# Kernel optimization log

Measured on AMD Instinct MI355X. Metric: run time of the kernel, lower is better.

The kernel has to match this reference:

```python
import jax, jax.numpy as jnp
import numpy as np
import math

B, S, D, H, L, F = 32, 512, 512, 8, 4, 2048
DK = D // H
EPS = 1e-5


def _cosine_pos_emb(seq_len, d_model):
    pe = np.zeros((seq_len, d_model), dtype=np.float32)
    position = np.arange(seq_len, dtype=np.float32)[:, None]
    div_term = np.exp(np.arange(0, d_model, 2, dtype=np.float32) * (-math.log(10000.0) / d_model))
    pe[:, 0::2] = np.sin(position * div_term)
    pe[:, 1::2] = np.cos(position * div_term)
    return jnp.asarray(pe[None])  # (1, S, D)


def setup_inputs() -> dict:
    key = jax.random.key(0)
    ks = jax.random.split(key, 12)
    w = 0.02
    return {
        "q_embed_data": jax.random.normal(ks[0], (B, S, D), jnp.float32),
        "qa_embed_data": jax.random.normal(ks[1], (B, S, D), jnp.float32),
        "forget_rate": jax.random.uniform(ks[2], (B, S, 1), jnp.float32),
        "pos_emb": _cosine_pos_emb(S, D),
        # per-layer stacked params (torch Linear convention: W is (out,in))
        "Wk": w * jax.random.normal(ks[3], (L, D, D), jnp.float32),
        "bk": jnp.zeros((L, D), jnp.float32),
        "Wv": w * jax.random.normal(ks[4], (L, D, D), jnp.float32),
        "bv": jnp.zeros((L, D), jnp.float32),
        "Wo": w * jax.random.normal(ks[5], (L, D, D), jnp.float32),
        "bo": jnp.zeros((L, D), jnp.float32),
        "W1": w * jax.random.normal(ks[6], (L, F, D), jnp.float32),
        "b1": jnp.zeros((L, F), jnp.float32),
        "W2": w * jax.random.normal(ks[7], (L, D, F), jnp.float32),
        "b2": jnp.zeros((L, D), jnp.float32),
        "ln1_g": jnp.ones((L, D), jnp.float32),
        "ln1_b": jnp.zeros((L, D), jnp.float32),
        "ln2_g": jnp.ones((L, D), jnp.float32),
        "ln2_b": jnp.zeros((L, D), jnp.float32),
    }


def _layer_norm(x, g, b):
    mu = jnp.mean(x, axis=-1, keepdims=True)
    var = jnp.mean(jnp.square(x - mu), axis=-1, keepdims=True)
    return (x - mu) * jax.lax.rsqrt(var + EPS) * g + b


def _forward(q_embed_data, qa_embed_data, forget_rate, pos_emb,
             Wk, bk, Wv, bv, Wo, bo, W1, b1, W2, b2,
             ln1_g, ln1_b, ln2_g, ln2_b):
    x = q_embed_data + pos_emb   # queries/keys stream
    y = qa_embed_data + pos_emb  # values stream (fixed across layers)
    scale = 1.0 / math.sqrt(DK)
    # mask=0 path: triu(k=0)==0 -> strictly past positions only (j < i)
    allowed = jnp.tril(jnp.ones((S, S), dtype=bool), k=-1)
    fr = forget_rate[:, None, :, :]  # (B,1,S,1): row-wise decay on scores
    neg = jnp.asarray(-1e32, x.dtype)

    def block(x, p):
        wk, bk_, wv, bv_, wo, bo_, w1, b1_, w2, b2_, g1, be1, g2, be2 = p
        # kq_same=1: q and k share the k_linear projection (so q == k here)
        kq = (jnp.einsum('bsd,ed->bse', x, wk) + bk_).reshape(B, S, H, DK).transpose(0, 2, 1, 3)
        v = (jnp.einsum('bsd,ed->bse', y, wv) + bv_).reshape(B, S, H, DK).transpose(0, 2, 1, 3)
        scores = jnp.einsum('bhsd,bhtd->bhst', kq, kq) * scale
        scores = scores * fr
        scores = jnp.where(allowed, scores, neg)
        attn = jax.nn.softmax(scores, axis=-1)
        attn = attn.at[:, :, 0, :].set(0.0)  # zero_pad: first query row zeroed
        ctx = jnp.einsum('bhst,bhtd->bhsd', attn, v).transpose(0, 2, 1, 3).reshape(B, S, D)
        out = jnp.einsum('bsd,ed->bse', ctx, wo) + bo_
        x = _layer_norm(x + out, g1, be1)
        ff = jnp.einsum('bsf,df->bsd', jax.nn.relu(jnp.einsum('bsd,fd->bsf', x, w1) + b1_), w2) + b2_
        x = _layer_norm(x + ff, g2, be2)
        return x, None

    x, _ = jax.lax.scan(block, x, (Wk, bk, Wv, bv, Wo, bo, W1, b1, W2, b2, ln1_g, ln1_b, ln2_g, ln2_b))
    return x


def reference(q_embed_data, qa_embed_data, forget_rate, pos_emb,
              Wk, bk, Wv, bv, Wo, bo, W1, b1, W2, b2,
              ln1_g, ln1_b, ln2_g, ln2_b):
    return _forward(q_embed_data, qa_embed_data, forget_rate, pos_emb,
                    Wk, bk, Wv, bv, Wo, bo, W1, b1, W2, b2,
                    ln1_g, ln1_b, ln2_g, ln2_b)
```

## Files before the change

### kernel.cpp

```cpp
#include <hip/hip_runtime.h>
#include <hip/hip_bf16.h>

constexpr int B_ = 32, S_ = 512, D_ = 512, H_ = 8, L_ = 4, F_ = 2048, DK_ = 64;

typedef __attribute__((ext_vector_type(8))) short short8;
typedef __attribute__((ext_vector_type(4))) float f32x4;

__device__ inline unsigned short f2b(float f) {
  union { __hip_bfloat16 h; unsigned short u; } cv;
  cv.h = __float2bfloat16(f);
  return cv.u;
}
__device__ inline float b2f(unsigned short u) {
  union { unsigned int i; float f; } c;
  c.i = ((unsigned int)u) << 16;
  return c.f;
}
__device__ inline float waveReduceSum(float v) {
  #pragma unroll
  for (int o = 32; o > 0; o >>= 1) v += __shfl_xor(v, o);
  return v;
}

__global__ void prep_kernel(const float4* __restrict__ q, const float4* __restrict__ qa,
                            const float4* __restrict__ pos, float4* __restrict__ xf,
                            uint2* __restrict__ xb, uint2* __restrict__ yb) {
  int i = blockIdx.x * blockDim.x + threadIdx.x;
  float4 p = pos[i & 65535];
  float4 a = q[i], c = qa[i];
  float4 xv, yv;
  xv.x = a.x + p.x; xv.y = a.y + p.y; xv.z = a.z + p.z; xv.w = a.w + p.w;
  yv.x = c.x + p.x; yv.y = c.y + p.y; yv.z = c.z + p.z; yv.w = c.w + p.w;
  xf[i] = xv;
  uint2 px, py;
  px.x = (unsigned)f2b(xv.x) | ((unsigned)f2b(xv.y) << 16);
  px.y = (unsigned)f2b(xv.z) | ((unsigned)f2b(xv.w) << 16);
  py.x = (unsigned)f2b(yv.x) | ((unsigned)f2b(yv.y) << 16);
  py.y = (unsigned)f2b(yv.z) | ((unsigned)f2b(yv.w) << 16);
  xb[i] = px;
  yb[i] = py;
}

__global__ void cast_kernel(const float4* __restrict__ src, uint2* __restrict__ dst, int n4) {
  int i = blockIdx.x * blockDim.x + threadIdx.x;
  if (i >= n4) return;
  float4 v = src[i];
  uint2 p;
  p.x = (unsigned)f2b(v.x) | ((unsigned)f2b(v.y) << 16);
  p.y = (unsigned)f2b(v.z) | ((unsigned)f2b(v.w) << 16);
  dst[i] = p;
}

template<int RELU, int STORE>
__global__ __launch_bounds__(256, 2) void gemm128_kernel(
    const __hip_bfloat16* __restrict__ A,
    const __hip_bfloat16* __restrict__ W,
    const float* __restrict__ bias,
    const __hip_bfloat16* __restrict__ A2,
    const __hip_bfloat16* __restrict__ W2,
    const float* __restrict__ bias2,
    __hip_bfloat16* __restrict__ Cb,
    __hip_bfloat16* __restrict__ Cb2,
    int Ndim, int Kdim, int kLen)
{
  __shared__ char lds[32768];
  const int tid = threadIdx.x, wave = tid >> 6, lane = tid & 63;
  const int rl = lane & 15, gq = lane >> 4;
  const int wr = wave >> 1, wc = wave & 1;

  const int nwg = gridDim.x * gridDim.y;
  const int lin = blockIdx.y * gridDim.x + blockIdx.x;
  const int swz = (lin & 7) * (nwg >> 3) + (lin >> 3);
  const int bx = swz % gridDim.x, by = swz / gridDim.x;

  const int row0 = by * 128;
  const int col0 = bx * 128;

  const __hip_bfloat16* Ap = A;
  const __hip_bfloat16* Wp = W;
  const float* bp = bias;
  int kOff = blockIdx.z * kLen;
  if (STORE == 3) {
    kOff = 0;
    if (blockIdx.z) { Ap = A2; Wp = W2; bp = bias2; }
  }

  f32x4 acc[4][4] = {};
  const int ntiles = kLen >> 5;

  auto stage = [&](int kt, int d) {
    const int kbase = kOff + (kt << 5);
    #pragma unroll
    for (int r = 0; r < 2; ++r) {
      int p = r * 4096 + tid * 16;
      int R = p >> 6, c = (p >> 4) & 3;
      int gc = c ^ ((R >> 1) & 3);
      const __hip_bfloat16* srcA = Ap + (size_t)(row0 + R) * Kdim + kbase + gc * 8;
      __builtin_amdgcn_global_load_lds(
          (const __attribute__((address_space(1))) void*)srcA,
          (__attribute__((address_space(3))) void*)(lds + d * 8192 + p), 16, 0, 0);
      const __hip_bfloat16* srcW = Wp + (size_t)(col0 + R) * Kdim + kbase + gc * 8;
      __builtin_amdgcn_global_load_lds(
          (const __attribute__((address_space(1))) void*)srcW,
          (__attribute__((address_space(3))) void*)(lds + 16384 + d * 8192 + p), 16, 0, 0);
    }
  };

  stage(0, 0);
  __syncthreads();
  for (int kt = 0; kt < ntiles; ++kt) {
    const int d = kt & 1;
    if (kt + 1 < ntiles) stage(kt + 1, d ^ 1);

    short8 aF[4], bF[4];
    #pragma unroll
    for (int m = 0; m < 4; ++m) {
      int rr = wr * 64 + m * 16 + rl;
      aF[m] = *(const short8*)(lds + d * 8192 + rr * 64 + ((gq ^ ((rr >> 1) & 3)) << 4));
    }
    #pragma unroll
    for (int n = 0; n < 4; ++n) {
      int rr = wc * 64 + n * 16 + rl;
      bF[n] = *(const short8*)(lds + 16384 + d * 8192 + rr * 64 + ((gq ^ ((rr >> 1) & 3)) << 4));
    }
    __builtin_amdgcn_s_setprio(1);
    #pragma unroll
    for (int m = 0; m < 4; ++m)
      #pragma unroll
      for (int n = 0; n < 4; ++n)
        acc[m][n] = __builtin_amdgcn_mfma_f32_16x16x32_bf16(aF[m], bF[n], acc[m][n], 0, 0, 0);
    __builtin_amdgcn_s_setprio(0);
    __syncthreads();
  }

  char* sw = lds + wave * 8192;
  const bool vt = (STORE == 3) && (blockIdx.z == 1);
  const bool addb = (STORE == 3) ? true : ((bias != nullptr) && (blockIdx.z == 0));
  float bvv[4];
  #pragma unroll
  for (int n = 0; n < 4; ++n)
    bvv[n] = addb ? bp[col0 + wc * 64 + n * 16 + rl] : 0.0f;

  #pragma unroll
  for (int n = 0; n < 4; ++n)
    #pragma unroll
    for (int m = 0; m < 4; ++m)
      #pragma unroll
      for (int j = 0; j < 4; ++j) {
        float val = acc[m][n][j] + bvv[n];
        if (RELU) val = fmaxf(val, 0.0f);
        int addr;
        if (vt) {
          int orow = n * 16 + rl, ocol = m * 16 + gq * 4 + j;
          addr = orow * 128 + ((ocol * 2) ^ ((orow & 7) << 4));
        } else {
          int orow = m * 16 + gq * 4 + j;
          addr = orow * 128 + (((n * 16 + rl) * 2) ^ (((orow >> 1) & 7) << 4));
        }
        *(unsigned short*)(sw + addr) = f2b(val);
      }
  asm volatile("s_waitcnt lgkmcnt(0)" ::: "memory");
  __builtin_amdgcn_sched_barrier(0);

  __hip_bfloat16* Cbd = blockIdx.z ? Cb2 : Cb;
  const int cchunk = lane & 7;
  if (vt) {
    const int bh64 = ((row0 >> 9) * 8 + (col0 >> 6) + wc) * 64;
    const int tbase = (row0 & 511) + wr * 64;
    #pragma unroll
    for (int it = 0; it < 8; ++it) {
      int d0 = it * 8 + (lane >> 3);
      uint4 vv = *(const uint4*)(sw + d0 * 128 + ((cchunk * 16) ^ ((d0 & 7) << 4)));
      *(uint4*)((char*)Cbd + ((size_t)(bh64 + d0) * 512 + tbase) * 2 + cchunk * 16) = vv;
    }
  } else {
    #pragma unroll
    for (int it = 0; it < 8; ++it) {
      int orow = it * 8 + (lane >> 3);
      uint4 vv = *(const uint4*)(sw + orow * 128 + ((cchunk * 16) ^ (((orow >> 1) & 7) << 4)));
      *(uint4*)((char*)Cbd + ((size_t)(row0 + wr * 64 + orow) * Ndim + col0 + wc * 64) * 2 +
                cchunk * 16) = vv;
    }
  }
}

__global__ __launch_bounds__(256, 2) void fattn_kernel(
    const __hip_bfloat16* __restrict__ kq,
    const __hip_bfloat16* __restrict__ vT,
    const float* __restrict__ fr,
    __hip_bfloat16* __restrict__ ctx)
{
  __shared__ char lds[40960];
  const int tid = threadIdx.x, wave = tid >> 6, lane = tid & 63;
  const int rl = lane & 15, gq = lane >> 4;
  const int lin = blockIdx.x;
  const int qb = (3 - (lin >> 8)) * 128;
  const int wpi = lin & 255;
  const int bh = (wpi & 7) * 32 + (wpi >> 3);
  const int b = bh >> 3, h = bh & 7;
  const size_t kqbase = ((size_t)b * S_) * D_ + h * DK_;
  const size_t vtbase = ((size_t)bh * DK_) * S_;
  const int qw0 = qb + wave * 32;
  const int qw_end = qw0 + 32;

  short8 qA[2][2];
  #pragma unroll
  for (int qf = 0; qf < 2; ++qf)
    #pragma unroll
    for (int kf = 0; kf < 2; ++kf)
      qA[qf][kf] = *(const short8*)(kq + kqbase + (size_t)(qw0 + qf * 16 + rl) * D_ + kf * 32 + gq * 8);

  float sfv[2][4];
  #pragma unroll
  for (int qf = 0; qf < 2; ++qf)
    #pragma unroll
    for (int j = 0; j < 4; ++j)
      sfv[qf][j] = fr[b * S_ + qw0 + qf * 16 + gq * 4 + j] * 0.125f;

  f32x4 o[2][4] = {};
  float mrow[2][4], lrow[2][4];
  #pragma unroll
  for (int qf = 0; qf < 2; ++qf)
    #pragma unroll
    for (int j = 0; j < 4; ++j) { mrow[qf][j] = -3.0e38f; lrow[qf][j] = 0.0f; }

  int sgoff[2], sldsoff[2];
  #pragma unroll
  for (int c = 0; c < 2; ++c) {
    int p = (wave * 2 + c) * 1024 + lane * 16;
    int r = p >> 7;
    int ch = (p >> 4) & 7;
    sgoff[c] = r * 1024 + ((ch ^ (r & 7)) << 4);
    sldsoff[c] = (wave * 2 + c) * 1024;
  }
  const char* kgbase = (const char*)kq + kqbase * 2;
  const char* vgbase = (const char*)vT + vtbase * 2;

  auto stage = [&](int ti, int d) {
    const int t0 = ti << 6;
    #pragma unroll
    for (int c = 0; c < 2; ++c) {
      __builtin_amdgcn_global_load_lds(
          (const __attribute__((address_space(1))) void*)(kgbase + (size_t)t0 * 1024 + sgoff[c]),
          (__attribute__((address_space(3))) void*)(lds + d * 8192 + sldsoff[c]), 16, 0, 0);
      __builtin_amdgcn_global_load_lds(
          (const __attribute__((address_space(1))) void*)(vgbase + t0 * 2 + sgoff[c]),
          (__attribute__((address_space(3))) void*)(lds + 16384 + d * 8192 + sldsoff[c]), 16, 0, 0);
    }
  };

  const int nt = (qb + 128) >> 6;
  stage(0, 0);
  for (int ti = 0; ti < nt; ++ti) {
    const int t0 = ti << 6;
    const int d = ti & 1;
    if (ti + 1 < nt) {
      stage(ti + 1, d ^ 1);
      asm volatile("s_waitcnt vmcnt(4)" ::: "memory");
    } else {
      asm volatile("s_waitcnt vmcnt(0)" ::: "memory");
    }
    __builtin_amdgcn_sched_barrier(0);
    __builtin_amdgcn_s_barrier();
    __builtin_amdgcn_sched_barrier(0);

    if (t0 < qw_end) {
      short8 kB[4][2];
      #pragma unroll
      for (int tf = 0; tf < 4; ++tf)
        #pragma unroll
        for (int kf = 0; kf < 2; ++kf) {
          int r = tf * 16 + rl;
          kB[tf][kf] = *(const short8*)(lds + d * 8192 + r * 128 + (((kf * 4 + gq) ^ (r & 7)) << 4));
        }
      short8 vB[4][2];
      #pragma unroll
      for (int df = 0; df < 4; ++df)
        #pragma unroll
        for (int kf = 0; kf < 2; ++kf) {
          int r = df * 16 + rl;
          vB[df][kf] = *(const short8*)(lds + 16384 + d * 8192 + r * 128 + (((kf * 4 + gq) ^ (r & 7)) << 4));
        }

      #pragma unroll
      for (int qf = 0; qf < 2; ++qf) {
        f32x4 c4[4] = {};
        #pragma unroll
        for (int tf = 0; tf < 4; ++tf)
          #pragma unroll
          for (int kf = 0; kf < 2; ++kf)
            c4[tf] = __builtin_amdgcn_mfma_f32_16x16x32_bf16(qA[qf][kf], kB[tf][kf], c4[tf], 0, 0, 0);

        const int qg0 = qw0 + qf * 16 + gq * 4;
        #pragma unroll
        for (int tf = 0; tf < 4; ++tf) {
          int tg = t0 + tf * 16 + rl;
          #pragma unroll
          for (int j = 0; j < 4; ++j) {
            float s = c4[tf][j] * sfv[qf][j];
            c4[tf][j] = (tg >= qg0 + j) ? -3.0e38f : s;
          }
        }
        float tm[4];
        #pragma unroll
        for (int j = 0; j < 4; ++j) {
          tm[j] = fmaxf(fmaxf(c4[0][j], c4[1][j]), fmaxf(c4[2][j], c4[3][j]));
          #pragma unroll
          for (int msk = 1; msk < 16; msk <<= 1) tm[j] = fmaxf(tm[j], __shfl_xor(tm[j], msk));
        }
        #pragma unroll
        for (int j = 0; j < 4; ++j) {
          float mn = fmaxf(mrow[qf][j], tm[j]);
          float fac = __expf(mrow[qf][j] - mn);
          mrow[qf][j] = mn;
          lrow[qf][j] *= fac;
          #pragma unroll
          for (int df = 0; df < 4; ++df) o[qf][df][j] *= fac;
        }
        float rs[4] = {0.f, 0.f, 0.f, 0.f};
        #pragma unroll
        for (int tf = 0; tf < 4; ++tf) {
          int tloc = tf * 16 + rl;
          #pragma unroll
          for (int j = 0; j < 4; ++j) {
            float e = __expf(c4[tf][j] - mrow[qf][j]);
            rs[j] += e;
            int qloc = gq * 4 + j;
            int addr = 32768 + wave * 2048 + qloc * 128 +
                       ((((tloc >> 3) ^ (qloc & 7)) << 4)) + (tloc & 7) * 2;
            *(unsigned short*)(lds + addr) = f2b(e);
          }
        }
        #pragma unroll
        for (int j = 0; j < 4; ++j) {
          float r = rs[j];
          #pragma unroll
          for (int msk = 1; msk < 16; msk <<= 1) r += __shfl_xor(r, msk);
          lrow[qf][j] += r;
        }
        asm volatile("s_waitcnt lgkmcnt(0)" ::: "memory");
        __builtin_amdgcn_sched_barrier(0);
        short8 pA[2];
        #pragma unroll
        for (int kf = 0; kf < 2; ++kf)
          pA[kf] = *(const short8*)(lds + 32768 + wave * 2048 + rl * 128 +
                                    (((kf * 4 + gq) ^ (rl & 7)) << 4));
        #pragma unroll
        for (int df = 0; df < 4; ++df)
          #pragma unroll
          for (int kf = 0; kf < 2; ++kf)
            o[qf][df] = __builtin_amdgcn_mfma_f32_16x16x32_bf16(pA[kf], vB[df][kf], o[qf][df], 0, 0, 0);
      }
    }
    __builtin_amdgcn_sched_barrier(0);
    __builtin_amdgcn_s_barrier();
    __builtin_amdgcn_sched_barrier(0);
  }

  #pragma unroll
  for (int qf = 0; qf < 2; ++qf)
    #pragma unroll
    for (int j = 0; j < 4; ++j) {
      int qg = qw0 + qf * 16 + gq * 4 + j;
      float inv = (qg == 0) ? 0.0f : 1.0f / lrow[qf][j];
      #pragma unroll
      for (int df = 0; df < 4; ++df) {
        union { __hip_bfloat16 hh; unsigned short u; } cv;
        cv.u = f2b(o[qf][df][j] * inv);
        ctx[((size_t)(b * S_ + qg)) * D_ + h * DK_ + df * 16 + rl] = cv.hh;
      }
    }
}

template<int NADD>
__global__ __launch_bounds__(256) void ln_kernel(
    const float4* __restrict__ xin, const uint4* __restrict__ add,
    const uint4* __restrict__ add2,
    const float* __restrict__ g, const float* __restrict__ bta,
    float4* xf_out, uint2* __restrict__ xb_out)
{
  const int lane = threadIdx.x & 63, wv = threadIdx.x >> 6;
  const size_t row = (size_t)blockIdx.x * 4 + wv;
  const size_t base4 = row * 128;

  float4 x0 = xin[base4 + lane * 2], x1 = xin[base4 + lane * 2 + 1];
  uint4 ab = add[row * 64 + lane];
  const unsigned short* ap = (const unsigned short*)&ab;
  float v[8];
  v[0] = x0.x; v[1] = x0.y; v[2] = x0.z; v[3] = x0.w;
  v[4] = x1.x; v[5] = x1.y; v[6] = x1.z; v[7] = x1.w;
  #pragma unroll
  for (int i = 0; i < 8; ++i) v[i] += b2f(ap[i]);
  if (NADD == 2) {
    uint4 ab2 = add2[row * 64 + lane];
    const unsigned short* ap2 = (const unsigned short*)&ab2;
    #pragma unroll
    for (int i = 0; i < 8; ++i) v[i] += b2f(ap2[i]);
  }
  float s = 0.0f;
  #pragma unroll
  for (int i = 0; i < 8; ++i) s += v[i];
  s = waveReduceSum(s);
  float mu = s * (1.0f / 512.0f);
  float vs = 0.0f;
  #pragma unroll
  for (int i = 0; i < 8; ++i) { float dd = v[i] - mu; vs += dd * dd; }
  vs = waveReduceSum(vs);
  float rstd = rsqrtf(vs * (1.0f / 512.0f) + 1e-5f);

  const int c0i = lane * 8;
  float4 gg0 = *(const float4*)(g + c0i), gg1 = *(const float4*)(g + c0i + 4);
  float4 bb0 = *(const float4*)(bta + c0i), bb1 = *(const float4*)(bta + c0i + 4);
  float o[8];
  o[0] = (v[0] - mu) * rstd * gg0.x + bb0.x;
  o[1] = (v[1] - mu) * rstd * gg0.y + bb0.y;
  o[2] = (v[2] - mu) * rstd * gg0.z + bb0.z;
  o[3] = (v[3] - mu) * rstd * gg0.w + bb0.w;
  o[4] = (v[4] - mu) * rstd * gg1.x + bb1.x;
  o[5] = (v[5] - mu) * rstd * gg1.y + bb1.y;
  o[6] = (v[6] - mu) * rstd * gg1.z + bb1.z;
  o[7] = (v[7] - mu) * rstd * gg1.w + bb1.w;
  float4 w0, w1;
  w0.x = o[0]; w0.y = o[1]; w0.z = o[2]; w0.w = o[3];
  w1.x = o[4]; w1.y = o[5]; w1.z = o[6]; w1.w = o[7];
  xf_out[base4 + lane * 2] = w0;
  xf_out[base4 + lane * 2 + 1] = w1;
  uint2 p0, p1;
  p0.x = (unsigned)f2b(o[0]) | ((unsigned)f2b(o[1]) << 16);
  p0.y = (unsigned)f2b(o[2]) | ((unsigned)f2b(o[3]) << 16);
  p1.x = (unsigned)f2b(o[4]) | ((unsigned)f2b(o[5]) << 16);
  p1.y = (unsigned)f2b(o[6]) | ((unsigned)f2b(o[7]) << 16);
  xb_out[row * 128 + lane * 2] = p0;
  xb_out[row * 128 + lane * 2 + 1] = p1;
}

extern "C" void kernel_launch(void* const* d_in, const int* in_sizes, int n_in,
                              void* d_out, int out_size, void* d_ws, size_t ws_size,
                              hipStream_t stream) {
  (void)in_sizes; (void)n_in; (void)out_size; (void)ws_size;
  const float* q   = (const float*)d_in[0];
  const float* qa  = (const float*)d_in[1];
  const float* frr = (const float*)d_in[2];
  const float* pos = (const float*)d_in[3];
  const float* Wk  = (const float*)d_in[4];
  const float* bk  = (const float*)d_in[5];
  const float* Wv  = (const float*)d_in[6];
  const float* bv  = (const float*)d_in[7];
  const float* Wo  = (const float*)d_in[8];
  const float* bo  = (const float*)d_in[9];
  const float* W1  = (const float*)d_in[10];
  const float* b1  = (const float*)d_in[11];
  const float* W2  = (const float*)d_in[12];
  const float* b2  = (const float*)d_in[13];
  const float* g1  = (const float*)d_in[14];
  const float* be1 = (const float*)d_in[15];
  const float* g2  = (const float*)d_in[16];
  const float* be2 = (const float*)d_in[17];

  char* ws = (char*)d_ws;
  float*          xf   = (float*)(ws + 0);
  __hip_bfloat16* xb   = (__hip_bfloat16*)(ws + 33554432);
  __hip_bfloat16* yb   = (__hip_bfloat16*)(ws + 50331648);
  __hip_bfloat16* kqb  = (__hip_bfloat16*)(ws + 67108864);
  __hip_bfloat16* vtb  = (__hip_bfloat16*)(ws + 83886080);
  __hip_bfloat16* ctxb = (__hip_bfloat16*)(ws + 100663296);
  __hip_bfloat16* hb   = (__hip_bfloat16*)(ws + 117440512);
  __hip_bfloat16* wkb  = (__hip_bfloat16*)(ws + 184549376);
  __hip_bfloat16* wvb  = (__hip_bfloat16*)(ws + 186646528);
  __hip_bfloat16* wob  = (__hip_bfloat16*)(ws + 188743680);
  __hip_bfloat16* w1b  = (__hip_bfloat16*)(ws + 190840832);
  __hip_bfloat16* w2b  = (__hip_bfloat16*)(ws + 199229440);
  __hip_bfloat16* obf = (__hip_bfloat16*)(ws + 67108864);
  __hip_bfloat16* pf0 = (__hip_bfloat16*)(ws + 83886080);
  __hip_bfloat16* pf1 = (__hip_bfloat16*)(ws + 100663296);

  prep_kernel<<<8192, 256, 0, stream>>>((const float4*)q, (const float4*)qa,
                                        (const float4*)pos, (float4*)xf,
                                        (uint2*)xb, (uint2*)yb);
  cast_kernel<<<1024, 256, 0, stream>>>((const float4*)Wk, (uint2*)wkb, 262144);
  cast_kernel<<<1024, 256, 0, stream>>>((const float4*)Wv, (uint2*)wvb, 262144);
  cast_kernel<<<1024, 256, 0, stream>>>((const float4*)Wo, (uint2*)wob, 262144);
  cast_kernel<<<4096, 256, 0, stream>>>((const float4*)W1, (uint2*)w1b, 1048576);
  cast_kernel<<<4096, 256, 0, stream>>>((const float4*)W2, (uint2*)w2b, 1048576);

  for (int l = 0; l < L_; ++l) {
    gemm128_kernel<0,3><<<dim3(4, 128, 2), 256, 0, stream>>>(
        xb, wkb + (size_t)l * 262144, bk + l * 512,
        yb, wvb + (size_t)l * 262144, bv + l * 512,
        kqb, vtb, 512, 512, 512);
    fattn_kernel<<<1024, 256, 0, stream>>>(kqb, vtb, frr, ctxb);
    gemm128_kernel<0,0><<<dim3(4, 128, 1), 256, 0, stream>>>(
        ctxb, wob + (size_t)l * 262144, bo + l * 512,
        nullptr, nullptr, nullptr, obf, nullptr, 512, 512, 512);
    ln_kernel<1><<<4096, 256, 0, stream>>>((const float4*)xf, (const uint4*)obf, nullptr,
                                           g1 + l * 512, be1 + l * 512,
                                           (float4*)xf, (uint2*)xb);
    gemm128_kernel<1,0><<<dim3(16, 128, 1), 256, 0, stream>>>(
        xb, w1b + (size_t)l * 1048576, b1 + l * 2048,
        nullptr, nullptr, nullptr, hb, nullptr, 2048, 512, 512);
    gemm128_kernel<0,0><<<dim3(4, 128, 2), 256, 0, stream>>>(
        hb, w2b + (size_t)l * 1048576, b2 + l * 512,
        nullptr, nullptr, nullptr, pf0, pf1, 512, 2048, 1024);
    float* lnout = (l == L_ - 1) ? (float*)d_out : xf;
    ln_kernel<2><<<4096, 256, 0, stream>>>((const float4*)xf, (const uint4*)pf0,
                                           (const uint4*)pf1,
                                           g2 + l * 512, be2 + l * 512,
                                           (float4*)lnout, (uint2*)xb);
  }
}
```

Before: 848.6 us.

## Load full per-head K and V into LDS and drop per-tile staging barriers

Each attention block now handles one (batch, head) half with 8 waves and loads that head's whole K and V (128 KB) into LDS once. The double-buffered per-tile staging and the block barriers inside the key loop are gone, and queries are read from LDS instead of global memory. Waves are assigned query strips in a mirrored order so that short and long causal rows share a block. The change removes repeated staging and synchronisation. In exchange, the 144 KB LDS footprint limits each CU to one block, so occupancy drops. All loads also happen up front with no overlap against compute, and the lower-query block loads K and V rows it never uses.

```diff
diff --git a/kernel.cpp b/kernel.cpp
--- a/kernel.cpp
+++ b/kernel.cpp
@@ -184,31 +184,43 @@
   }
 }
 
-__global__ __launch_bounds__(256, 2) void fattn_kernel(
+__global__ __launch_bounds__(512, 2) void fattn_kernel(
     const __hip_bfloat16* __restrict__ kq,
     const __hip_bfloat16* __restrict__ vT,
     const float* __restrict__ fr,
     __hip_bfloat16* __restrict__ ctx)
 {
-  __shared__ char lds[40960];
+  __shared__ char lds[147456];
   const int tid = threadIdx.x, wave = tid >> 6, lane = tid & 63;
   const int rl = lane & 15, gq = lane >> 4;
-  const int lin = blockIdx.x;
-  const int qb = (3 - (lin >> 8)) * 128;
-  const int wpi = lin & 255;
-  const int bh = (wpi & 7) * 32 + (wpi >> 3);
+  const int bh = blockIdx.x & 255;
+  const int blk = blockIdx.x >> 8;
   const int b = bh >> 3, h = bh & 7;
   const size_t kqbase = ((size_t)b * S_) * D_ + h * DK_;
   const size_t vtbase = ((size_t)bh * DK_) * S_;
-  const int qw0 = qb + wave * 32;
-  const int qw_end = qw0 + 32;
-
-  short8 qA[2][2];
-  #pragma unroll
-  for (int qf = 0; qf < 2; ++qf)
-    #pragma unroll
-    for (int kf = 0; kf < 2; ++kf)
-      qA[qf][kf] = *(const short8*)(kq + kqbase + (size_t)(qw0 + qf * 16 + rl) * D_ + kf * 32 + gq * 8);
+  const char* kg = (const char*)kq + kqbase * 2;
+  const char* vg = (const char*)vT + vtbase * 2;
+
+  #pragma unroll
+  for (int i = 0; i < 8; ++i) {
+    int p = i * 8192 + tid * 16;
+    int r = p >> 7, ch = (p >> 4) & 7;
+    __builtin_amdgcn_global_load_lds(
+        (const __attribute__((address_space(1))) void*)(kg + (size_t)r * 1024 + ((ch ^ (r & 7)) << 4)),
+        (__attribute__((address_space(3))) void*)(lds + p), 16, 0, 0);
+  }
+  #pragma unroll
+  for (int i = 0; i < 8; ++i) {
+    int p = i * 8192 + tid * 16;
+    int d = p >> 10, ck = (p >> 4) & 63;
+    __builtin_amdgcn_global_load_lds(
+        (const __attribute__((address_space(1))) void*)(vg + (size_t)d * 1024 + ((ck ^ (d & 7)) << 4)),
+        (__attribute__((address_space(3))) void*)(lds + 65536 + p), 16, 0, 0);
+  }
+
+  const int qidx = blk * 8 + (wave < 4 ? wave : 11 - wave);
+  const int qw0 = qidx * 32;
+  const int nt = (qidx >> 1) + 1;
 
   float sfv[2][4];
   #pragma unroll
@@ -217,6 +229,19 @@
     for (int j = 0; j < 4; ++j)
       sfv[qf][j] = fr[b * S_ + qw0 + qf * 16 + gq * 4 + j] * 0.125f;
 
+  asm volatile("s_waitcnt vmcnt(0)" ::: "memory");
+  __builtin_amdgcn_sched_barrier(0);
+  __builtin_amdgcn_s_barrier();
+
+  short8 qA[2][2];
+  #pragma unroll
+  for (int qf = 0; qf < 2; ++qf)
+    #pragma unroll
+    for (int kf = 0; kf < 2; ++kf) {
+      int r = qw0 + qf * 16 + rl;
+      qA[qf][kf] = *(const short8*)(lds + r * 128 + (((kf * 4 + gq) ^ (r & 7)) << 4));
+    }
+
   f32x4 o[2][4] = {};
   float mrow[2][4], lrow[2][4];
   #pragma unroll
@@ -224,137 +249,95 @@
     #pragma unroll
     for (int j = 0; j < 4; ++j) { mrow[qf][j] = -3.0e38f; lrow[qf][j] = 0.0f; }
 
-  int sgoff[2], sldsoff[2];
-  #pragma unroll
-  for (int c = 0; c < 2; ++c) {
-    int p = (wave * 2 + c) * 1024 + lane * 16;
-    int r = p >> 7;
-    int ch = (p >> 4) & 7;
-    sgoff[c] = r * 1024 + ((ch ^ (r & 7)) << 4);
-    sldsoff[c] = (wave * 2 + c) * 1024;
-  }
-  const char* kgbase = (const char*)kq + kqbase * 2;
-  const char* vgbase = (const char*)vT + vtbase * 2;
-
-  auto stage = [&](int ti, int d) {
-    const int t0 = ti << 6;
-    #pragma unroll
-    for (int c = 0; c < 2; ++c) {
-      __builtin_amdgcn_global_load_lds(
-          (const __attribute__((address_space(1))) void*)(kgbase + (size_t)t0 * 1024 + sgoff[c]),
-          (__attribute__((address_space(3))) void*)(lds + d * 8192 + sldsoff[c]), 16, 0, 0);
-      __builtin_amdgcn_global_load_lds(
-          (const __attribute__((address_space(1))) void*)(vgbase + t0 * 2 + sgoff[c]),
-          (__attribute__((address_space(3))) void*)(lds + 16384 + d * 8192 + sldsoff[c]), 16, 0, 0);
-    }
-  };
-
-  const int nt = (qb + 128) >> 6;
-  stage(0, 0);
+  char* pbase = lds + 131072 + wave * 2048;
+
   for (int ti = 0; ti < nt; ++ti) {
     const int t0 = ti << 6;
-    const int d = ti & 1;
-    if (ti + 1 < nt) {
-      stage(ti + 1, d ^ 1);
-      asm volatile("s_waitcnt vmcnt(4)" ::: "memory");
-    } else {
-      asm volatile("s_waitcnt vmcnt(0)" ::: "memory");
-    }
-    __builtin_amdgcn_sched_barrier(0);
-    __builtin_amdgcn_s_barrier();
-    __builtin_amdgcn_sched_barrier(0);
-
-    if (t0 < qw_end) {
-      short8 kB[4][2];
+    short8 kB[4][2];
+    #pragma unroll
+    for (int tf = 0; tf < 4; ++tf)
+      #pragma unroll
+      for (int kf = 0; kf < 2; ++kf) {
+        int r = t0 + tf * 16 + rl;
+        kB[tf][kf] = *(const short8*)(lds + r * 128 + (((kf * 4 + gq) ^ (r & 7)) << 4));
+      }
+    short8 vB[4][2];
+    #pragma unroll
+    for (int df = 0; df < 4; ++df)
+      #pragma unroll
+      for (int kf = 0; kf < 2; ++kf) {
+        int d = df * 16 + rl;
+        vB[df][kf] = *(const short8*)(lds + 65536 + d * 1024 +
+                                      ((8 * ti + ((kf * 4 + gq) ^ (d & 7))) << 4));
+      }
+
+    #pragma unroll
+    for (int qf = 0; qf < 2; ++qf) {
+      f32x4 c4[4] = {};
       #pragma unroll
       for (int tf = 0; tf < 4; ++tf)
         #pragma unroll
-        for (int kf = 0; kf < 2; ++kf) {
-          int r = tf * 16 + rl;
-          kB[tf][kf] = *(const short8*)(lds + d * 8192 + r * 128 + (((kf * 4 + gq) ^ (r & 7)) << 4));
+        for (int kf = 0; kf < 2; ++kf)
+          c4[tf] = __builtin_amdgcn_mfma_f32_16x16x32_bf16(qA[qf][kf], kB[tf][kf], c4[tf], 0, 0, 0);
+
+      const int qg0 = qw0 + qf * 16 + gq * 4;
+      #pragma unroll
+      for (int tf = 0; tf < 4; ++tf) {
+        int tg = t0 + tf * 16 + rl;
+        #pragma unroll
+        for (int j = 0; j < 4; ++j) {
+          float s = c4[tf][j] * sfv[qf][j];
+          c4[tf][j] = (tg >= qg0 + j) ? -3.0e38f : s;
         }
-      short8 vB[4][2];
+      }
+      float tm[4];
+      #pragma unroll
+      for (int j = 0; j < 4; ++j) {
+        tm[j] = fmaxf(fmaxf(c4[0][j], c4[1][j]), fmaxf(c4[2][j], c4[3][j]));
+        #pragma unroll
+        for (int msk = 1; msk < 16; msk <<= 1) tm[j] = fmaxf(tm[j], __shfl_xor(tm[j], msk));
+      }
+      #pragma unroll
+      for (int j = 0; j < 4; ++j) {
+        float mn = fmaxf(mrow[qf][j], tm[j]);
+        float fac = __expf(mrow[qf][j] - mn);
+        mrow[qf][j] = mn;
+        lrow[qf][j] *= fac;
+        #pragma unroll
+        for (int df = 0; df < 4; ++df) o[qf][df][j] *= fac;
+      }
+      float rs[4] = {0.f, 0.f, 0.f, 0.f};
+      #pragma unroll
+      for (int tf = 0; tf < 4; ++tf) {
+        int tloc = tf * 16 + rl;
+        #pragma unroll
+        for (int j = 0; j < 4; ++j) {
+          float e = __expf(c4[tf][j] - mrow[qf][j]);
+          rs[j] += e;
+          int qloc = gq * 4 + j;
+          int addr = qloc * 128 + ((((tloc >> 3) ^ (qloc & 7)) << 4)) + (tloc & 7) * 2;
+          *(unsigned short*)(pbase + addr) = f2b(e);
+        }
+      }
+      #pragma unroll
+      for (int j = 0; j < 4; ++j) {
+        float r = rs[j];
+        #pragma unroll
+        for (int msk = 1; msk < 16; msk <<= 1) r += __shfl_xor(r, msk);
+        lrow[qf][j] += r;
+      }
+      asm volatile("s_waitcnt lgkmcnt(0)" ::: "memory");
+      __builtin_amdgcn_sched_barrier(0);
+      short8 pA[2];
+      #pragma unroll
+      for (int kf = 0; kf < 2; ++kf)
+        pA[kf] = *(const short8*)(pbase + rl * 128 + (((kf * 4 + gq) ^ (rl & 7)) << 4));
       #pragma unroll
       for (int df = 0; df < 4; ++df)
         #pragma unroll
-        for (int kf = 0; kf < 2; ++kf) {
-          int r = df * 16 + rl;
-          vB[df][kf] = *(const short8*)(lds + 16384 + d * 8192 + r * 128 + (((kf * 4 + gq) ^ (r & 7)) << 4));
-        }
-
-      #pragma unroll
-      for (int qf = 0; qf < 2; ++qf) {
-        f32x4 c4[4] = {};
-        #pragma unroll
-        for (int tf = 0; tf < 4; ++tf)
-          #pragma unroll
-          for (int kf = 0; kf < 2; ++kf)
-            c4[tf] = __builtin_amdgcn_mfma_f32_16x16x32_bf16(qA[qf][kf], kB[tf][kf], c4[tf], 0, 0, 0);
-
-        const int qg0 = qw0 + qf * 16 + gq * 4;
-        #pragma unroll
-        for (int tf = 0; tf < 4; ++tf) {
-          int tg = t0 + tf * 16 + rl;
-          #pragma unroll
-          for (int j = 0; j < 4; ++j) {
-            float s = c4[tf][j] * sfv[qf][j];
-            c4[tf][j] = (tg >= qg0 + j) ? -3.0e38f : s;
-          }
-        }
-        float tm[4];
-        #pragma unroll
-        for (int j = 0; j < 4; ++j) {
-          tm[j] = fmaxf(fmaxf(c4[0][j], c4[1][j]), fmaxf(c4[2][j], c4[3][j]));
-          #pragma unroll
-          for (int msk = 1; msk < 16; msk <<= 1) tm[j] = fmaxf(tm[j], __shfl_xor(tm[j], msk));
-        }
-        #pragma unroll
-        for (int j = 0; j < 4; ++j) {
-          float mn = fmaxf(mrow[qf][j], tm[j]);
-          float fac = __expf(mrow[qf][j] - mn);
-          mrow[qf][j] = mn;
-          lrow[qf][j] *= fac;
-          #pragma unroll
-          for (int df = 0; df < 4; ++df) o[qf][df][j] *= fac;
-        }
-        float rs[4] = {0.f, 0.f, 0.f, 0.f};
-        #pragma unroll
-        for (int tf = 0; tf < 4; ++tf) {
-          int tloc = tf * 16 + rl;
-          #pragma unroll
-          for (int j = 0; j < 4; ++j) {
-            float e = __expf(c4[tf][j] - mrow[qf][j]);
-            rs[j] += e;
-            int qloc = gq * 4 + j;
-            int addr = 32768 + wave * 2048 + qloc * 128 +
-                       ((((tloc >> 3) ^ (qloc & 7)) << 4)) + (tloc & 7) * 2;
-            *(unsigned short*)(lds + addr) = f2b(e);
-          }
-        }
-        #pragma unroll
-        for (int j = 0; j < 4; ++j) {
-          float r = rs[j];
-          #pragma unroll
-          for (int msk = 1; msk < 16; msk <<= 1) r += __shfl_xor(r, msk);
-          lrow[qf][j] += r;
-        }
-        asm volatile("s_waitcnt lgkmcnt(0)" ::: "memory");
-        __builtin_amdgcn_sched_barrier(0);
-        short8 pA[2];
-        #pragma unroll
         for (int kf = 0; kf < 2; ++kf)
-          pA[kf] = *(const short8*)(lds + 32768 + wave * 2048 + rl * 128 +
-                                    (((kf * 4 + gq) ^ (rl & 7)) << 4));
-        #pragma unroll
-        for (int df = 0; df < 4; ++df)
-          #pragma unroll
-          for (int kf = 0; kf < 2; ++kf)
-            o[qf][df] = __builtin_amdgcn_mfma_f32_16x16x32_bf16(pA[kf], vB[df][kf], o[qf][df], 0, 0, 0);
-      }
-    }
-    __builtin_amdgcn_sched_barrier(0);
-    __builtin_amdgcn_s_barrier();
-    __builtin_amdgcn_sched_barrier(0);
+          o[qf][df] = __builtin_amdgcn_mfma_f32_16x16x32_bf16(pA[kf], vB[df][kf], o[qf][df], 0, 0, 0);
+    }
   }
 
   #pragma unroll
@@ -488,7 +471,7 @@
         xb, wkb + (size_t)l * 262144, bk + l * 512,
         yb, wvb + (size_t)l * 262144, bv + l * 512,
         kqb, vtb, 512, 512, 512);
-    fattn_kernel<<<1024, 256, 0, stream>>>(kqb, vtb, frr, ctxb);
+    fattn_kernel<<<512, 512, 0, stream>>>(kqb, vtb, frr, ctxb);
     gemm128_kernel<0,0><<<dim3(4, 128, 1), 256, 0, stream>>>(
         ctxb, wob + (size_t)l * 262144, bo + l * 512,
         nullptr, nullptr, nullptr, obf, nullptr, 512, 512, 512);
```

New measurement: 854.2 us. Within noise of the previous version (+0.7%).
